# Kernel optimization log

Measured on AMD Instinct MI355X. Metric: run time of the kernel, lower is better.

Reference implementation:

```python
import jax, jax.numpy as jnp
import numpy as np

B, S, H, I = 2, 2048, 4096, 16384
EPS = 1e-12


def setup_inputs() -> dict:
    key = jax.random.key(0)
    ks = jax.random.split(key, 8)
    w_scale = 0.02
    return {
        "input": jax.random.normal(ks[0], (B, S, H), jnp.float32),
        "residual": jax.random.normal(ks[1], (B, S, H), jnp.float32),
        "bias": jax.random.normal(ks[2], (H,), jnp.float32) * w_scale,
        "attn_nw": jnp.ones((H,), jnp.float32),
        "attn_nb": jnp.zeros((H,), jnp.float32),
        "inter_w": jax.random.normal(ks[3], (I, H), jnp.float32) * w_scale,
        "inter_b": jax.random.normal(ks[4], (I,), jnp.float32) * w_scale,
        "output_w": jax.random.normal(ks[5], (H, I), jnp.float32) * w_scale,
        "output_b": jax.random.normal(ks[6], (H,), jnp.float32) * w_scale,
    }


def reference(input, residual, bias, attn_nw, attn_nb, inter_w, inter_b, output_w, output_b):
    # Fused mlp_gemm: residual_add = input + residual + attn-output bias
    residual_add = input + residual + bias  # [B,S,H]
    # LayerNorm over hidden dim with attn_nw/attn_nb
    mean = jnp.mean(residual_add, axis=-1, keepdims=True)
    var = jnp.var(residual_add, axis=-1, keepdims=True)
    ln = (residual_add - mean) * jax.lax.rsqrt(var + EPS) * attn_nw + attn_nb
    # Intermediate GEMM + bias + GELU (DeepSpeed uses tanh-approx gelu)
    inter = jax.nn.gelu(jnp.einsum("bsh,ih->bsi", ln, inter_w) + inter_b, approximate=True)
    # Output projection (vector_matmul)
    out = jnp.einsum("bsi,hi->bsh", inter, output_w)
    # bias_residual: add residual_add and output bias
    return out + residual_add + output_b
```

## Files before the change

kernel.cpp:

```cpp
#include <hip/hip_runtime.h>
#include <hip/hip_bf16.h>
#include <cstdint>
#include <math.h>

typedef __attribute__((ext_vector_type(4))) float f32x4;
typedef __attribute__((ext_vector_type(8))) __bf16 bf16x8;

__device__ __forceinline__ unsigned short f2bf(float f) {
    union { float f; unsigned u; } v; v.f = f;
    unsigned u = v.u + 0x7fffu + ((v.u >> 16) & 1u);
    return (unsigned short)(u >> 16);
}

__device__ __forceinline__ float gelu_tanh(float x) {
    float x3 = x * x * x;
    float t = tanhf(0.7978845608028654f * (x + 0.044715f * x3));
    return 0.5f * x * (1.0f + t);
}

__device__ __forceinline__ void gload_lds16(const void* g, void* l) {
    __builtin_amdgcn_global_load_lds(
        (__attribute__((address_space(1))) void*)(uintptr_t)g,
        (__attribute__((address_space(3))) void*)(unsigned)(uintptr_t)l,
        16, 0, 0);
}

__global__ __launch_bounds__(256)
void fused_add_ln(const float* __restrict__ in, const float* __restrict__ res,
                  const float* __restrict__ bias, const float* __restrict__ nw,
                  const float* __restrict__ nb, float* __restrict__ resadd,
                  unsigned short* __restrict__ lnout, int H) {
    const int row = blockIdx.x;
    const int tid = threadIdx.x;
    const size_t base = (size_t)row * H;
    float v[16];
    float s = 0.f, ss = 0.f;
#pragma unroll
    for (int i = 0; i < 4; ++i) {
        int idx = (i * 256 + tid) * 4;
        float4 a = *(const float4*)(in + base + idx);
        float4 b = *(const float4*)(res + base + idx);
        float4 c = *(const float4*)(bias + idx);
        float x0 = a.x + b.x + c.x, x1 = a.y + b.y + c.y;
        float x2 = a.z + b.z + c.z, x3 = a.w + b.w + c.w;
        v[i * 4 + 0] = x0; v[i * 4 + 1] = x1; v[i * 4 + 2] = x2; v[i * 4 + 3] = x3;
        s += x0 + x1 + x2 + x3;
        ss += x0 * x0 + x1 * x1 + x2 * x2 + x3 * x3;
    }
#pragma unroll
    for (int off = 32; off > 0; off >>= 1) {
        s += __shfl_down(s, off);
        ss += __shfl_down(ss, off);
    }
    __shared__ float red[8];
    const int w = tid >> 6;
    if ((tid & 63) == 0) { red[w] = s; red[4 + w] = ss; }
    __syncthreads();
    s = red[0] + red[1] + red[2] + red[3];
    ss = red[4] + red[5] + red[6] + red[7];
    const float mean = s / H;
    const float var = ss / H - mean * mean;
    const float rstd = rsqrtf(var + 1e-12f);
#pragma unroll
    for (int i = 0; i < 4; ++i) {
        int idx = (i * 256 + tid) * 4;
        float4 wv = *(const float4*)(nw + idx);
        float4 bv = *(const float4*)(nb + idx);
        float4 r;
        r.x = v[i * 4 + 0]; r.y = v[i * 4 + 1]; r.z = v[i * 4 + 2]; r.w = v[i * 4 + 3];
        *(float4*)(resadd + base + idx) = r;
        ushort4 o;
        o.x = f2bf((r.x - mean) * rstd * wv.x + bv.x);
        o.y = f2bf((r.y - mean) * rstd * wv.y + bv.y);
        o.z = f2bf((r.z - mean) * rstd * wv.z + bv.z);
        o.w = f2bf((r.w - mean) * rstd * wv.w + bv.w);
        *(ushort4*)(lnout + base + idx) = o;
    }
}

__global__ __launch_bounds__(256)
void cast_w(const float* __restrict__ w, unsigned short* __restrict__ o, long long n4) {
    long long i = (long long)blockIdx.x * 256 + threadIdx.x;
    if (i >= n4) return;
    float4 f = *(const float4*)(w + i * 4);
    ushort4 u;
    u.x = f2bf(f.x); u.y = f2bf(f.y); u.z = f2bf(f.z); u.w = f2bf(f.w);
    *(ushort4*)(o + i * 4) = u;
}

#define GBM 256
#define GBN 256
#define GBK 64

#define STAGE(s, mat, h, T) do {                                              \
    const unsigned short* _src = ((mat) ? pB : pA)                            \
        + (size_t)((h) * 128) * K + (size_t)(T) * 64;                         \
    char* _dst = ldsc + (s) * 65536 + (mat) * 32768 + (h) * 16384 + dOff;     \
    gload_lds16(_src, _dst);                                                  \
    gload_lds16(_src + (size_t)64 * K, _dst + 8192);                          \
} while (0)

#define RD_B(s) do {                                                          \
    _Pragma("unroll")                                                         \
    for (int ni = 0; ni < 4; ++ni)                                            \
        _Pragma("unroll")                                                     \
        for (int kk = 0; kk < 2; ++kk)                                        \
            bq[ni][kk] = *(const bf16x8*)(ldsc + (s) * 65536 + 32768          \
                + ((wc * 64 + ni * 16 + lrow) << 7) + ckk[kk]);               \
} while (0)

#define RD_A(q, s) do {                                                       \
    _Pragma("unroll")                                                         \
    for (int m2 = 0; m2 < 2; ++m2)                                            \
        _Pragma("unroll")                                                     \
        for (int kk = 0; kk < 2; ++kk)                                        \
            aq[m2][kk] = *(const bf16x8*)(ldsc + (s) * 65536                  \
                + ((wr * 128 + ((q) * 2 + m2) * 16 + lrow) << 7) + ckk[kk]);  \
} while (0)

#define BAR asm volatile("s_barrier" ::: "memory")
#define GATE4 asm volatile("s_waitcnt vmcnt(4)" ::: "memory")
#define GATE0 asm volatile("s_waitcnt vmcnt(0)" ::: "memory")
#define NOGATE

#define PHASE(q, s, STG, GT) do {                                             \
    if ((q) == 0) RD_B(s);                                                    \
    RD_A(q, s);                                                               \
    STG;                                                                      \
    GT;                                                                       \
    BAR;                                                                      \
    asm volatile("s_waitcnt lgkmcnt(0)" ::: "memory");                        \
    __builtin_amdgcn_sched_barrier(0);                                        \
    __builtin_amdgcn_s_setprio(1);                                            \
    _Pragma("unroll")                                                         \
    for (int m2 = 0; m2 < 2; ++m2)                                            \
        _Pragma("unroll")                                                     \
        for (int ni = 0; ni < 4; ++ni)                                        \
            _Pragma("unroll")                                                 \
            for (int kk = 0; kk < 2; ++kk)                                    \
                acc[(q) * 2 + m2][ni] = __builtin_amdgcn_mfma_f32_16x16x32_bf16( \
                    aq[m2][kk], bq[ni][kk], acc[(q) * 2 + m2][ni], 0, 0, 0);  \
    __builtin_amdgcn_s_setprio(0);                                            \
    BAR;                                                                      \
} while (0)

template <int EPI>
__global__ __launch_bounds__(512, 2)
void gemm256(const unsigned short* __restrict__ A,
             const unsigned short* __restrict__ B,
             const float* __restrict__ bias_n,
             const float* __restrict__ resadd,
             void* __restrict__ Cout,
             int M, int N, int K) {
    __shared__ unsigned short lds[2][2][2][128 * 64];
    char* ldsc = (char*)&lds[0][0][0][0];
    const int tid = threadIdx.x;
    const int lane = tid & 63;
    const int w = tid >> 6;
    const int wr = w >> 2;
    const int wc = w & 3;

    const int nwg = gridDim.x;
    const int lg = (blockIdx.x & 7) * (nwg >> 3) + (blockIdx.x >> 3);
    const int nbx = N / GBN;
    const int brow = lg / nbx;
    const int bcol = lg % nbx;

    const int srow = tid >> 3;
    const int scol = ((((tid & 7) << 4) ^ ((srow & 7) << 4)) >> 1);
    const unsigned short* pA = A + (size_t)(brow * GBM + srow) * K + scol;
    const unsigned short* pB = B + (size_t)(bcol * GBN + srow) * K + scol;
    const int dOff = tid * 16;

    const int lrow = lane & 15;
    int ckk[2];
    ckk[0] = (((lane >> 4) << 4)) ^ ((lrow & 7) << 4);
    ckk[1] = ckk[0] ^ 64;

    f32x4 acc[8][4] = {};
    bf16x8 aq[2][2];
    bf16x8 bq[4][2];

    const int NT = K / GBK;
    const int niter = NT / 2;

    STAGE(0, 1, 0, 0); STAGE(0, 1, 1, 0);
    STAGE(0, 0, 0, 0); STAGE(0, 0, 1, 0);
    STAGE(1, 1, 0, 1); STAGE(1, 1, 1, 1);
    GATE4;
    BAR;

    for (int i = 0; i < niter - 1; ++i) {
        const int T0 = 2 * i, T1 = 2 * i + 1;
        PHASE(0, 0, STAGE(1, 0, 0, T1),     NOGATE);
        PHASE(1, 0, STAGE(1, 0, 1, T1),     NOGATE);
        PHASE(2, 0, STAGE(0, 1, 0, T0 + 2), NOGATE);
        PHASE(3, 0, STAGE(0, 1, 1, T0 + 2), GATE4);
        PHASE(0, 1, STAGE(0, 0, 0, T0 + 2), NOGATE);
        PHASE(1, 1, STAGE(0, 0, 1, T0 + 2), NOGATE);
        PHASE(2, 1, STAGE(1, 1, 0, T1 + 2), NOGATE);
        PHASE(3, 1, STAGE(1, 1, 1, T1 + 2), GATE4);
    }
    {
        const int T1 = NT - 1;
        PHASE(0, 0, STAGE(1, 0, 0, T1), NOGATE);
        PHASE(1, 0, STAGE(1, 0, 1, T1), NOGATE);
        PHASE(2, 0, NOGATE,             NOGATE);
        PHASE(3, 0, NOGATE,             GATE0);
        PHASE(0, 1, NOGATE,             NOGATE);
        PHASE(1, 1, NOGATE,             NOGATE);
        PHASE(2, 1, NOGATE,             NOGATE);
        PHASE(3, 1, NOGATE,             NOGATE);
    }

    const int c0 = bcol * GBN + wc * 64 + lrow;
    const int r0 = brow * GBM + wr * 128 + (lane >> 4) * 4;
#pragma unroll
    for (int mi = 0; mi < 8; ++mi) {
#pragma unroll
        for (int j = 0; j < 4; ++j) {
            const int row = r0 + mi * 16 + j;
#pragma unroll
            for (int ni = 0; ni < 4; ++ni) {
                const int col = c0 + ni * 16;
                float x = acc[mi][ni][j] + bias_n[col];
                if (EPI == 0) {
                    ((unsigned short*)Cout)[(size_t)row * N + col] = f2bf(gelu_tanh(x));
                } else {
                    const size_t off = (size_t)row * N + col;
                    ((float*)Cout)[off] = x + resadd[off];
                }
            }
        }
    }
}

extern "C" void kernel_launch(void* const* d_in, const int* in_sizes, int n_in,
                              void* d_out, int out_size, void* d_ws, size_t ws_size,
                              hipStream_t stream) {
    const float* input    = (const float*)d_in[0];
    const float* residual = (const float*)d_in[1];
    const float* bias     = (const float*)d_in[2];
    const float* attn_nw  = (const float*)d_in[3];
    const float* attn_nb  = (const float*)d_in[4];
    const float* inter_w  = (const float*)d_in[5];
    const float* inter_b  = (const float*)d_in[6];
    const float* output_w = (const float*)d_in[7];
    const float* output_b = (const float*)d_in[8];

    const int H = in_sizes[3];
    const int I = in_sizes[6];
    const int T = in_sizes[0] / H;

    char* ws = (char*)d_ws;
    float* resadd      = (float*)ws;
    unsigned short* ln = (unsigned short*)(ws + (size_t)T * H * 4);
    unsigned short* w1 = (unsigned short*)((char*)ln + (size_t)T * H * 2);
    unsigned short* w2 = w1 + (size_t)I * H;
    unsigned short* act = w2 + (size_t)H * I;

    fused_add_ln<<<T, 256, 0, stream>>>(input, residual, bias, attn_nw, attn_nb,
                                        resadd, ln, H);

    {
        long long n4 = (long long)I * H / 4;
        int blocks = (int)((n4 + 255) / 256);
        cast_w<<<blocks, 256, 0, stream>>>(inter_w, w1, n4);
        cast_w<<<blocks, 256, 0, stream>>>(output_w, w2, n4);
    }

    {
        dim3 grid((T / GBM) * (I / GBN));
        gemm256<0><<<grid, 512, 0, stream>>>(ln, w1, inter_b, nullptr, act, T, I, H);
    }

    {
        dim3 grid((T / GBM) * (H / GBN));
        gemm256<1><<<grid, 512, 0, stream>>>(act, w2, output_b, resadd, d_out, T, H, I);
    }
}
```

Before: 1.120 ms.

## Double-buffer A-fragment LDS reads to overlap them with MFMA phases

```diff
diff --git a/kernel.cpp b/kernel.cpp
--- a/kernel.cpp
+++ b/kernel.cpp
@@ -109,28 +109,16 @@
                 + ((wc * 64 + ni * 16 + lrow) << 7) + ckk[kk]);               \
 } while (0)
 
-#define RD_A(q, s) do {                                                       \
+#define RD_A(bank, q, s) do {                                                 \
     _Pragma("unroll")                                                         \
     for (int m2 = 0; m2 < 2; ++m2)                                            \
         _Pragma("unroll")                                                     \
         for (int kk = 0; kk < 2; ++kk)                                        \
-            aq[m2][kk] = *(const bf16x8*)(ldsc + (s) * 65536                  \
+            aq[bank][m2][kk] = *(const bf16x8*)(ldsc + (s) * 65536            \
                 + ((wr * 128 + ((q) * 2 + m2) * 16 + lrow) << 7) + ckk[kk]);  \
 } while (0)
 
-#define BAR asm volatile("s_barrier" ::: "memory")
-#define GATE4 asm volatile("s_waitcnt vmcnt(4)" ::: "memory")
-#define GATE0 asm volatile("s_waitcnt vmcnt(0)" ::: "memory")
-#define NOGATE
-
-#define PHASE(q, s, STG, GT) do {                                             \
-    if ((q) == 0) RD_B(s);                                                    \
-    RD_A(q, s);                                                               \
-    STG;                                                                      \
-    GT;                                                                       \
-    BAR;                                                                      \
-    asm volatile("s_waitcnt lgkmcnt(0)" ::: "memory");                        \
-    __builtin_amdgcn_sched_barrier(0);                                        \
+#define MF(q, bank) do {                                                      \
     __builtin_amdgcn_s_setprio(1);                                            \
     _Pragma("unroll")                                                         \
     for (int m2 = 0; m2 < 2; ++m2)                                            \
@@ -139,10 +127,18 @@
             _Pragma("unroll")                                                 \
             for (int kk = 0; kk < 2; ++kk)                                    \
                 acc[(q) * 2 + m2][ni] = __builtin_amdgcn_mfma_f32_16x16x32_bf16( \
-                    aq[m2][kk], bq[ni][kk], acc[(q) * 2 + m2][ni], 0, 0, 0);  \
+                    aq[bank][m2][kk], bq[ni][kk], acc[(q) * 2 + m2][ni], 0, 0, 0); \
     __builtin_amdgcn_s_setprio(0);                                            \
-    BAR;                                                                      \
-} while (0)
+} while (0)
+
+#define BAR asm volatile("s_barrier" ::: "memory")
+#define GATE4 asm volatile("s_waitcnt vmcnt(4)" ::: "memory")
+#define GATE0 asm volatile("s_waitcnt vmcnt(0)" ::: "memory")
+#define LG4 do { asm volatile("s_waitcnt lgkmcnt(4)" ::: "memory");           \
+                 __builtin_amdgcn_sched_barrier(0); } while (0)
+#define LG0 do { asm volatile("s_waitcnt lgkmcnt(0)" ::: "memory");           \
+                 __builtin_amdgcn_sched_barrier(0); } while (0)
+#define SB0 __builtin_amdgcn_sched_barrier(0)
 
 template <int EPI>
 __global__ __launch_bounds__(512, 2)
@@ -178,7 +174,7 @@
     ckk[1] = ckk[0] ^ 64;
 
     f32x4 acc[8][4] = {};
-    bf16x8 aq[2][2];
+    bf16x8 aq[2][2][2];
     bf16x8 bq[4][2];
 
     const int NT = K / GBK;
@@ -189,28 +185,44 @@
     STAGE(1, 1, 0, 1); STAGE(1, 1, 1, 1);
     GATE4;
     BAR;
+    RD_A(0, 0, 0);
 
     for (int i = 0; i < niter - 1; ++i) {
         const int T0 = 2 * i, T1 = 2 * i + 1;
-        PHASE(0, 0, STAGE(1, 0, 0, T1),     NOGATE);
-        PHASE(1, 0, STAGE(1, 0, 1, T1),     NOGATE);
-        PHASE(2, 0, STAGE(0, 1, 0, T0 + 2), NOGATE);
-        PHASE(3, 0, STAGE(0, 1, 1, T0 + 2), GATE4);
-        PHASE(0, 1, STAGE(0, 0, 0, T0 + 2), NOGATE);
-        PHASE(1, 1, STAGE(0, 0, 1, T0 + 2), NOGATE);
-        PHASE(2, 1, STAGE(1, 1, 0, T1 + 2), NOGATE);
-        PHASE(3, 1, STAGE(1, 1, 1, T1 + 2), GATE4);
+        RD_B(0); SB0; RD_A(1, 1, 0); STAGE(1, 0, 0, T1);
+        BAR; LG4; MF(0, 0); BAR;
+        RD_A(0, 2, 0); STAGE(1, 0, 1, T1);
+        BAR; LG4; MF(1, 1); BAR;
+        RD_A(1, 3, 0); STAGE(0, 1, 0, T0 + 2);
+        BAR; LG4; MF(2, 0); BAR;
+        STAGE(0, 1, 1, T0 + 2); GATE4;
+        BAR; RD_A(0, 0, 1); LG4; MF(3, 1); BAR;
+        RD_B(1); SB0; RD_A(1, 1, 1); STAGE(0, 0, 0, T0 + 2);
+        BAR; LG4; MF(0, 0); BAR;
+        RD_A(0, 2, 1); STAGE(0, 0, 1, T0 + 2);
+        BAR; LG4; MF(1, 1); BAR;
+        RD_A(1, 3, 1); STAGE(1, 1, 0, T1 + 2);
+        BAR; LG4; MF(2, 0); BAR;
+        STAGE(1, 1, 1, T1 + 2); GATE4;
+        BAR; RD_A(0, 0, 0); LG4; MF(3, 1); BAR;
     }
     {
         const int T1 = NT - 1;
-        PHASE(0, 0, STAGE(1, 0, 0, T1), NOGATE);
-        PHASE(1, 0, STAGE(1, 0, 1, T1), NOGATE);
-        PHASE(2, 0, NOGATE,             NOGATE);
-        PHASE(3, 0, NOGATE,             GATE0);
-        PHASE(0, 1, NOGATE,             NOGATE);
-        PHASE(1, 1, NOGATE,             NOGATE);
-        PHASE(2, 1, NOGATE,             NOGATE);
-        PHASE(3, 1, NOGATE,             NOGATE);
+        RD_B(0); SB0; RD_A(1, 1, 0); STAGE(1, 0, 0, T1);
+        BAR; LG4; MF(0, 0); BAR;
+        RD_A(0, 2, 0); STAGE(1, 0, 1, T1);
+        BAR; LG4; MF(1, 1); BAR;
+        RD_A(1, 3, 0);
+        BAR; LG4; MF(2, 0); BAR;
+        GATE0;
+        BAR; RD_A(0, 0, 1); LG4; MF(3, 1); BAR;
+        RD_B(1); SB0; RD_A(1, 1, 1);
+        BAR; LG4; MF(0, 0); BAR;
+        RD_A(0, 2, 1);
+        BAR; LG4; MF(1, 1); BAR;
+        RD_A(1, 3, 1);
+        BAR; LG4; MF(2, 0); BAR;
+        LG0; MF(3, 1);
     }
 
     const int c0 = bcol * GBN + wc * 64 + lrow;
```

Measured after the change: 1.360 ms. +21.4%, slower.

## Switch GEMM to 32x32x16 MFMA with register double-buffered LDS pipeline

Applied to the files above, without the earlier changes.

```diff
diff --git a/kernel.cpp b/kernel.cpp
--- a/kernel.cpp
+++ b/kernel.cpp
@@ -3,7 +3,7 @@
 #include <cstdint>
 #include <math.h>
 
-typedef __attribute__((ext_vector_type(4))) float f32x4;
+typedef __attribute__((ext_vector_type(16))) float f32x16;
 typedef __attribute__((ext_vector_type(8))) __bf16 bf16x8;
 
 __device__ __forceinline__ unsigned short f2bf(float f) {
@@ -90,7 +90,6 @@
 
 #define GBM 256
 #define GBN 256
-#define GBK 64
 
 #define STAGE(s, mat, h, T) do {                                              \
     const unsigned short* _src = ((mat) ? pB : pA)                            \
@@ -100,49 +99,35 @@
     gload_lds16(_src + (size_t)64 * K, _dst + 8192);                          \
 } while (0)
 
-#define RD_B(s) do {                                                          \
+#define STG(s, T) do { STAGE(s, 0, 0, T); STAGE(s, 0, 1, T);                  \
+                       STAGE(s, 1, 0, T); STAGE(s, 1, 1, T); } while (0)
+
+#define RD32(b, ks, s) do {                                                   \
     _Pragma("unroll")                                                         \
-    for (int ni = 0; ni < 4; ++ni)                                            \
-        _Pragma("unroll")                                                     \
-        for (int kk = 0; kk < 2; ++kk)                                        \
-            bq[ni][kk] = *(const bf16x8*)(ldsc + (s) * 65536 + 32768          \
-                + ((wc * 64 + ni * 16 + lrow) << 7) + ckk[kk]);               \
+    for (int m = 0; m < 4; ++m)                                               \
+        aq[b][m] = *(const bf16x8*)(ldsc + (s) * 65536                        \
+            + ((wr * 128 + m * 32 + l31) << 7) + ck[ks]);                     \
+    _Pragma("unroll")                                                         \
+    for (int n = 0; n < 2; ++n)                                               \
+        bq[b][n] = *(const bf16x8*)(ldsc + (s) * 65536 + 32768                \
+            + ((wc * 64 + n * 32 + l31) << 7) + ck[ks]);                      \
 } while (0)
 
-#define RD_A(q, s) do {                                                       \
-    _Pragma("unroll")                                                         \
-    for (int m2 = 0; m2 < 2; ++m2)                                            \
-        _Pragma("unroll")                                                     \
-        for (int kk = 0; kk < 2; ++kk)                                        \
-            aq[m2][kk] = *(const bf16x8*)(ldsc + (s) * 65536                  \
-                + ((wr * 128 + ((q) * 2 + m2) * 16 + lrow) << 7) + ckk[kk]);  \
-} while (0)
-
-#define BAR asm volatile("s_barrier" ::: "memory")
-#define GATE4 asm volatile("s_waitcnt vmcnt(4)" ::: "memory")
-#define GATE0 asm volatile("s_waitcnt vmcnt(0)" ::: "memory")
-#define NOGATE
-
-#define PHASE(q, s, STG, GT) do {                                             \
-    if ((q) == 0) RD_B(s);                                                    \
-    RD_A(q, s);                                                               \
-    STG;                                                                      \
-    GT;                                                                       \
-    BAR;                                                                      \
-    asm volatile("s_waitcnt lgkmcnt(0)" ::: "memory");                        \
-    __builtin_amdgcn_sched_barrier(0);                                        \
+#define MF32(b) do {                                                          \
     __builtin_amdgcn_s_setprio(1);                                            \
     _Pragma("unroll")                                                         \
-    for (int m2 = 0; m2 < 2; ++m2)                                            \
+    for (int m = 0; m < 4; ++m)                                               \
         _Pragma("unroll")                                                     \
-        for (int ni = 0; ni < 4; ++ni)                                        \
-            _Pragma("unroll")                                                 \
-            for (int kk = 0; kk < 2; ++kk)                                    \
-                acc[(q) * 2 + m2][ni] = __builtin_amdgcn_mfma_f32_16x16x32_bf16( \
-                    aq[m2][kk], bq[ni][kk], acc[(q) * 2 + m2][ni], 0, 0, 0);  \
+        for (int n = 0; n < 2; ++n)                                           \
+            acc[m][n] = __builtin_amdgcn_mfma_f32_32x32x16_bf16(              \
+                aq[b][m], bq[b][n], acc[m][n], 0, 0, 0);                      \
     __builtin_amdgcn_s_setprio(0);                                            \
-    BAR;                                                                      \
 } while (0)
+
+#define WAITP do { asm volatile("s_waitcnt lgkmcnt(0)" ::: "memory");         \
+                   __builtin_amdgcn_sched_barrier(0); } while (0)
+#define BAR   asm volatile("s_barrier" ::: "memory")
+#define GATE0 asm volatile("s_waitcnt vmcnt(0)" ::: "memory")
 
 template <int EPI>
 __global__ __launch_bounds__(512, 2)
@@ -152,8 +137,8 @@
              const float* __restrict__ resadd,
              void* __restrict__ Cout,
              int M, int N, int K) {
-    __shared__ unsigned short lds[2][2][2][128 * 64];
-    char* ldsc = (char*)&lds[0][0][0][0];
+    __shared__ unsigned short lds[2][2][256 * 64];
+    char* ldsc = (char*)&lds[0][0][0];
     const int tid = threadIdx.x;
     const int lane = tid & 63;
     const int w = tid >> 6;
@@ -172,58 +157,56 @@
     const unsigned short* pB = B + (size_t)(bcol * GBN + srow) * K + scol;
     const int dOff = tid * 16;
 
-    const int lrow = lane & 15;
-    int ckk[2];
-    ckk[0] = (((lane >> 4) << 4)) ^ ((lrow & 7) << 4);
-    ckk[1] = ckk[0] ^ 64;
-
-    f32x4 acc[8][4] = {};
-    bf16x8 aq[2][2];
-    bf16x8 bq[4][2];
-
-    const int NT = K / GBK;
+    const int l31 = lane & 31;
+    int ck[4];
+#pragma unroll
+    for (int ks = 0; ks < 4; ++ks)
+        ck[ks] = ((ks << 5) | (((lane >> 5) & 1) << 4)) ^ ((lane & 7) << 4);
+
+    f32x16 acc[4][2] = {};
+    bf16x8 aq[2][4];
+    bf16x8 bq[2][2];
+
+    const int NT = K / 64;
     const int niter = NT / 2;
 
-    STAGE(0, 1, 0, 0); STAGE(0, 1, 1, 0);
-    STAGE(0, 0, 0, 0); STAGE(0, 0, 1, 0);
-    STAGE(1, 1, 0, 1); STAGE(1, 1, 1, 1);
-    GATE4;
-    BAR;
+    STG(0, 0);
+    GATE0; BAR;
+    RD32(0, 0, 0);
 
     for (int i = 0; i < niter - 1; ++i) {
-        const int T0 = 2 * i, T1 = 2 * i + 1;
-        PHASE(0, 0, STAGE(1, 0, 0, T1),     NOGATE);
-        PHASE(1, 0, STAGE(1, 0, 1, T1),     NOGATE);
-        PHASE(2, 0, STAGE(0, 1, 0, T0 + 2), NOGATE);
-        PHASE(3, 0, STAGE(0, 1, 1, T0 + 2), GATE4);
-        PHASE(0, 1, STAGE(0, 0, 0, T0 + 2), NOGATE);
-        PHASE(1, 1, STAGE(0, 0, 1, T0 + 2), NOGATE);
-        PHASE(2, 1, STAGE(1, 1, 0, T1 + 2), NOGATE);
-        PHASE(3, 1, STAGE(1, 1, 1, T1 + 2), GATE4);
-    }
-    {
-        const int T1 = NT - 1;
-        PHASE(0, 0, STAGE(1, 0, 0, T1), NOGATE);
-        PHASE(1, 0, STAGE(1, 0, 1, T1), NOGATE);
-        PHASE(2, 0, NOGATE,             NOGATE);
-        PHASE(3, 0, NOGATE,             GATE0);
-        PHASE(0, 1, NOGATE,             NOGATE);
-        PHASE(1, 1, NOGATE,             NOGATE);
-        PHASE(2, 1, NOGATE,             NOGATE);
-        PHASE(3, 1, NOGATE,             NOGATE);
-    }
-
-    const int c0 = bcol * GBN + wc * 64 + lrow;
-    const int r0 = brow * GBM + wr * 128 + (lane >> 4) * 4;
-#pragma unroll
-    for (int mi = 0; mi < 8; ++mi) {
-#pragma unroll
-        for (int j = 0; j < 4; ++j) {
-            const int row = r0 + mi * 16 + j;
-#pragma unroll
-            for (int ni = 0; ni < 4; ++ni) {
-                const int col = c0 + ni * 16;
-                float x = acc[mi][ni][j] + bias_n[col];
+        const int Tn1 = 2 * i + 1, Tn2 = 2 * i + 2;
+        WAITP; MF32(0); RD32(1, 1, 0); STG(1, Tn1);
+        WAITP; MF32(1); RD32(0, 2, 0);
+        WAITP; MF32(0); RD32(1, 3, 0);
+        WAITP; MF32(1); GATE0; BAR; RD32(0, 0, 1);
+        WAITP; MF32(0); RD32(1, 1, 1); STG(0, Tn2);
+        WAITP; MF32(1); RD32(0, 2, 1);
+        WAITP; MF32(0); RD32(1, 3, 1);
+        WAITP; MF32(1); GATE0; BAR; RD32(0, 0, 0);
+    }
+    {
+        WAITP; MF32(0); RD32(1, 1, 0); STG(1, NT - 1);
+        WAITP; MF32(1); RD32(0, 2, 0);
+        WAITP; MF32(0); RD32(1, 3, 0);
+        WAITP; MF32(1); GATE0; BAR; RD32(0, 0, 1);
+        WAITP; MF32(0); RD32(1, 1, 1);
+        WAITP; MF32(1); RD32(0, 2, 1);
+        WAITP; MF32(0); RD32(1, 3, 1);
+        WAITP; MF32(1);
+    }
+
+    const int c0 = bcol * GBN + wc * 64 + l31;
+    const int r0 = brow * GBM + wr * 128 + ((lane >> 5) & 1) * 4;
+#pragma unroll
+    for (int m = 0; m < 4; ++m) {
+#pragma unroll
+        for (int reg = 0; reg < 16; ++reg) {
+            const int row = r0 + m * 32 + (reg & 3) + 8 * (reg >> 2);
+#pragma unroll
+            for (int n = 0; n < 2; ++n) {
+                const int col = c0 + n * 32;
+                float x = acc[m][n][reg] + bias_n[col];
                 if (EPI == 0) {
                     ((unsigned short*)Cout)[(size_t)row * N + col] = f2bf(gelu_tanh(x));
                 } else {
```

Result: slower. 1.279 ms (+14.1%).

## Restructure GEMM main loop with register double-buffering and fewer barriers

Applied to the files above, without the earlier changes.

```diff
diff --git a/kernel.cpp b/kernel.cpp
--- a/kernel.cpp
+++ b/kernel.cpp
@@ -90,7 +90,6 @@
 
 #define GBM 256
 #define GBN 256
-#define GBK 64
 
 #define STAGE(s, mat, h, T) do {                                              \
     const unsigned short* _src = ((mat) ? pB : pA)                            \
@@ -99,6 +98,9 @@
     gload_lds16(_src, _dst);                                                  \
     gload_lds16(_src + (size_t)64 * K, _dst + 8192);                          \
 } while (0)
+
+#define STG(s, T) do { STAGE(s, 0, 0, T); STAGE(s, 0, 1, T);                  \
+                       STAGE(s, 1, 0, T); STAGE(s, 1, 1, T); } while (0)
 
 #define RD_B(s) do {                                                          \
     _Pragma("unroll")                                                         \
@@ -109,28 +111,16 @@
                 + ((wc * 64 + ni * 16 + lrow) << 7) + ckk[kk]);               \
 } while (0)
 
-#define RD_A(q, s) do {                                                       \
+#define RD_A(bk, q, s) do {                                                   \
     _Pragma("unroll")                                                         \
     for (int m2 = 0; m2 < 2; ++m2)                                            \
         _Pragma("unroll")                                                     \
         for (int kk = 0; kk < 2; ++kk)                                        \
-            aq[m2][kk] = *(const bf16x8*)(ldsc + (s) * 65536                  \
+            aq[bk][m2][kk] = *(const bf16x8*)(ldsc + (s) * 65536              \
                 + ((wr * 128 + ((q) * 2 + m2) * 16 + lrow) << 7) + ckk[kk]);  \
 } while (0)
 
-#define BAR asm volatile("s_barrier" ::: "memory")
-#define GATE4 asm volatile("s_waitcnt vmcnt(4)" ::: "memory")
-#define GATE0 asm volatile("s_waitcnt vmcnt(0)" ::: "memory")
-#define NOGATE
-
-#define PHASE(q, s, STG, GT) do {                                             \
-    if ((q) == 0) RD_B(s);                                                    \
-    RD_A(q, s);                                                               \
-    STG;                                                                      \
-    GT;                                                                       \
-    BAR;                                                                      \
-    asm volatile("s_waitcnt lgkmcnt(0)" ::: "memory");                        \
-    __builtin_amdgcn_sched_barrier(0);                                        \
+#define MF(q, bk) do {                                                        \
     __builtin_amdgcn_s_setprio(1);                                            \
     _Pragma("unroll")                                                         \
     for (int m2 = 0; m2 < 2; ++m2)                                            \
@@ -139,10 +129,14 @@
             _Pragma("unroll")                                                 \
             for (int kk = 0; kk < 2; ++kk)                                    \
                 acc[(q) * 2 + m2][ni] = __builtin_amdgcn_mfma_f32_16x16x32_bf16( \
-                    aq[m2][kk], bq[ni][kk], acc[(q) * 2 + m2][ni], 0, 0, 0);  \
+                    aq[bk][m2][kk], bq[ni][kk], acc[(q) * 2 + m2][ni], 0, 0, 0); \
     __builtin_amdgcn_s_setprio(0);                                            \
-    BAR;                                                                      \
-} while (0)
+} while (0)
+
+#define WAITP do { asm volatile("s_waitcnt lgkmcnt(0)" ::: "memory");         \
+                   __builtin_amdgcn_sched_barrier(0); } while (0)
+#define BAR   asm volatile("s_barrier" ::: "memory")
+#define GATE0 asm volatile("s_waitcnt vmcnt(0)" ::: "memory")
 
 template <int EPI>
 __global__ __launch_bounds__(512, 2)
@@ -178,39 +172,36 @@
     ckk[1] = ckk[0] ^ 64;
 
     f32x4 acc[8][4] = {};
-    bf16x8 aq[2][2];
+    bf16x8 aq[2][2][2];
     bf16x8 bq[4][2];
 
-    const int NT = K / GBK;
+    const int NT = K / 64;
     const int niter = NT / 2;
 
-    STAGE(0, 1, 0, 0); STAGE(0, 1, 1, 0);
-    STAGE(0, 0, 0, 0); STAGE(0, 0, 1, 0);
-    STAGE(1, 1, 0, 1); STAGE(1, 1, 1, 1);
-    GATE4;
-    BAR;
+    STG(0, 0);
+    GATE0; BAR;
+    RD_B(0); RD_A(0, 0, 0);
 
     for (int i = 0; i < niter - 1; ++i) {
-        const int T0 = 2 * i, T1 = 2 * i + 1;
-        PHASE(0, 0, STAGE(1, 0, 0, T1),     NOGATE);
-        PHASE(1, 0, STAGE(1, 0, 1, T1),     NOGATE);
-        PHASE(2, 0, STAGE(0, 1, 0, T0 + 2), NOGATE);
-        PHASE(3, 0, STAGE(0, 1, 1, T0 + 2), GATE4);
-        PHASE(0, 1, STAGE(0, 0, 0, T0 + 2), NOGATE);
-        PHASE(1, 1, STAGE(0, 0, 1, T0 + 2), NOGATE);
-        PHASE(2, 1, STAGE(1, 1, 0, T1 + 2), NOGATE);
-        PHASE(3, 1, STAGE(1, 1, 1, T1 + 2), GATE4);
-    }
-    {
-        const int T1 = NT - 1;
-        PHASE(0, 0, STAGE(1, 0, 0, T1), NOGATE);
-        PHASE(1, 0, STAGE(1, 0, 1, T1), NOGATE);
-        PHASE(2, 0, NOGATE,             NOGATE);
-        PHASE(3, 0, NOGATE,             GATE0);
-        PHASE(0, 1, NOGATE,             NOGATE);
-        PHASE(1, 1, NOGATE,             NOGATE);
-        PHASE(2, 1, NOGATE,             NOGATE);
-        PHASE(3, 1, NOGATE,             NOGATE);
+        const int T1 = 2 * i + 1, T2 = 2 * i + 2;
+        WAITP; MF(0, 0); RD_A(1, 1, 0); STG(1, T1);
+        WAITP; MF(1, 1); RD_A(0, 2, 0);
+        WAITP; MF(2, 0); RD_A(1, 3, 0);
+        WAITP; MF(3, 1); GATE0; BAR; RD_B(1); RD_A(0, 0, 1);
+        WAITP; MF(0, 0); RD_A(1, 1, 1); STG(0, T2);
+        WAITP; MF(1, 1); RD_A(0, 2, 1);
+        WAITP; MF(2, 0); RD_A(1, 3, 1);
+        WAITP; MF(3, 1); GATE0; BAR; RD_B(0); RD_A(0, 0, 0);
+    }
+    {
+        WAITP; MF(0, 0); RD_A(1, 1, 0); STG(1, NT - 1);
+        WAITP; MF(1, 1); RD_A(0, 2, 0);
+        WAITP; MF(2, 0); RD_A(1, 3, 0);
+        WAITP; MF(3, 1); GATE0; BAR; RD_B(1); RD_A(0, 0, 1);
+        WAITP; MF(0, 0); RD_A(1, 1, 1);
+        WAITP; MF(1, 1); RD_A(0, 2, 1);
+        WAITP; MF(2, 0); RD_A(1, 3, 1);
+        WAITP; MF(3, 1);
     }
 
     const int c0 = bcol * GBN + wc * 64 + lrow;
```

After: 1.199 ms. +7.0%, slower.
